# Performance work log

Hardware: AMD Instinct MI355X
Metric: run time of the kernel (lower is better)

The kernel has to match this reference:

```python
import jax, jax.numpy as jnp
import numpy as np

# fp4 e2m1 representable magnitudes and rounding midpoints
FP4_LEVELS = jnp.array([0.0, 0.5, 1.0, 1.5, 2.0, 3.0, 4.0, 6.0], dtype=jnp.float32)
FP4_BOUNDS = jnp.array([0.25, 0.75, 1.25, 1.75, 2.5, 3.5, 5.0], dtype=jnp.float32)
EPS = 1e-8
RANK = 64      # activation_lowrank_svd
NITER = 2      # activation_lowrank_niter


def fp4_get_scalar(x):
    # per-tensor scale: amax / max_fp4e2m1 (6.0)
    return jnp.maximum(jnp.max(jnp.abs(x)) / 6.0, EPS)


def fp4_qdq(x):
    # quant (round-to-nearest fp4e2m1 grid) followed by rquant (dequant)
    s = fp4_get_scalar(x)
    y = x / s
    a = jnp.clip(jnp.abs(y), 0.0, 6.0)
    idx = jnp.searchsorted(FP4_BOUNDS, a)  # nearest-level index
    return jnp.sign(y) * FP4_LEVELS[idx] * s


def power_iter_svd(G, V0, niter):
    # Dion-style power iteration: G ~ U diag(S) V^T, V0: [n,k]
    V = V0
    U = None
    W = None
    for it in range(niter):
        P = G @ V                                  # [m,k]
        U, _ = jnp.linalg.qr(P)                    # reduced QR, U: [m,k]
        W = G.T @ U                                # [n,k]
        if it < niter - 1:
            V = W / (jnp.linalg.norm(W, axis=0, keepdims=True) + EPS)
    S = jnp.linalg.norm(W, axis=0)                 # [k]
    Vn = W / (S[None, :] + EPS)                    # [n,k]
    return U, S, Vn


def svd_quant(x2d, V0):
    # low-rank kernel + fp4-quantized factors + fp4-quantized residual
    U, S, V = power_iter_svd(x2d, V0, NITER)
    ug = U.T                                       # [k,m]
    vg = V.T                                       # [k,n]
    ker = (U * S[None, :]) @ vg                    # [m,n] full-precision kernel
    ugq = fp4_qdq(ug)
    vgq = fp4_qdq(vg)
    res_q = fp4_qdq(x2d - ker)                     # quantized residual
    return (ugq.T * S[None, :]) @ vgq + res_q      # reconstructed input


def setup_inputs() -> dict:
    key = jax.random.key(0)
    k1, k2, k3, k4 = jax.random.split(key, 4)
    B, Sq, Din, Dout, R = 4, 2048, 4096, 4096, RANK
    x = jax.random.normal(k1, (B, Sq, Din), jnp.float32)
    weight = jax.random.normal(k2, (Dout, Din), jnp.float32) * (1.0 / np.sqrt(Din))
    bias = jax.random.normal(k3, (Dout,), jnp.float32) * 0.01
    V0 = jax.random.normal(k4, (Din, R), jnp.float32)  # cached subspace (state)
    return {"x": x, "weight": weight, "bias": bias, "V0": V0}


def reference(x, weight, bias, V0):
    B, Sq, Din = x.shape
    # activation SVD + fp4 quantization on flattened [B*S, Din]
    xq = svd_quant(x.reshape(-1, Din), V0).reshape(B, Sq, Din)
    # weight fp4 quant/dequant
    wq = fp4_qdq(weight)
    return xq @ wq.T + bias
```

## Files before the change

kernel.cpp:

```cpp
#include <hip/hip_runtime.h>
#include <stdint.h>

#define EPSF 1e-8f
#define KT 4160

typedef float  f32x4  __attribute__((ext_vector_type(4)));
typedef __bf16 bf16x8 __attribute__((ext_vector_type(8)));
typedef __bf16 bf16x4 __attribute__((ext_vector_type(4)));

constexpr size_t oP    = 0;
constexpr size_t oW    = oP  + 8192*64;
constexpr size_t oG    = oW  + 4096*64;
constexpr size_t oM1   = oG  + 64*64;
constexpr size_t oScal = oM1 + 64*4096;
constexpr size_t nZero1= oScal + 4;
constexpr size_t nZero2= oG + 64*64;
constexpr size_t oS    = nZero1;
constexpr size_t oLinv = oS + 64;
constexpr size_t oV    = oLinv + 64*64;
constexpr size_t oU    = oV + 4096*64;
constexpr size_t endF32= oU + 8192*64;
constexpr size_t bfByte= ((endF32*4 + 255)/256)*256;
constexpr size_t oVq   = 0;
constexpr size_t oA    = oVq + 64*4096;
constexpr size_t oB    = oA + (size_t)8192*4160;
constexpr size_t oVcT  = oB + (size_t)4096*4160;
constexpr size_t oUT   = oVcT + 3*(size_t)64*4096;
constexpr size_t oUhl  = oUT + 3*(size_t)64*8192;
constexpr size_t oKVT  = oUhl + 2*(size_t)8192*64;
constexpr size_t endBF = oKVT + 2*(size_t)4096*64;
constexpr size_t WS_NEED = bfByte + endBF*2;

__device__ __forceinline__ float qlevel(float a){
  if (a <= 0.25f) return 0.0f;
  if (a <= 0.75f) return 0.5f;
  if (a <= 1.25f) return 1.0f;
  if (a <= 1.75f) return 1.5f;
  if (a <= 2.5f)  return 2.0f;
  if (a <= 3.5f)  return 3.0f;
  if (a <= 5.0f)  return 4.0f;
  return 6.0f;
}
__device__ __forceinline__ float qgrid(float v, float s){
  float y = v / s;
  float l = qlevel(fabsf(y));
  return y < 0.0f ? -l : l;
}

__global__ void k_zero(float* p, int n){
  for (int i = blockIdx.x*blockDim.x + threadIdx.x; i < n; i += gridDim.x*blockDim.x)
    p[i] = 0.0f;
}

__global__ void k_amax4(const float4* __restrict__ x, int n4, unsigned* __restrict__ out){
  float m = 0.f;
  for (int i = blockIdx.x*blockDim.x + threadIdx.x; i < n4; i += gridDim.x*blockDim.x){
    float4 v = x[i];
    m = fmaxf(m, fmaxf(fmaxf(fabsf(v.x), fabsf(v.y)), fmaxf(fabsf(v.z), fabsf(v.w))));
  }
  for (int o = 32; o > 0; o >>= 1) m = fmaxf(m, __shfl_down(m, o, 64));
  __shared__ float sm[4];
  int lane = threadIdx.x & 63, w = threadIdx.x >> 6;
  if (lane == 0) sm[w] = m;
  __syncthreads();
  if (threadIdx.x == 0)
    atomicMax(out, __float_as_uint(fmaxf(fmaxf(sm[0],sm[1]), fmaxf(sm[2],sm[3]))));
}

__global__ __launch_bounds__(256) void k_gv(
    float* __restrict__ P, const float* __restrict__ x,
    const __bf16* __restrict__ Bh, const __bf16* __restrict__ Bm, const __bf16* __restrict__ Bl){
  int m0 = blockIdx.x * 128;
  int d0 = blockIdx.y * 512;
  int lane = threadIdx.x & 63, wave = threadIdx.x >> 6;
  int kgrp = lane >> 4, lrow = lane & 15;
  f32x4 acc[2][4] = {};
  for (int dc = d0; dc < d0 + 512; dc += 32){
    bf16x8 ah[2], am[2], al[2];
    #pragma unroll
    for (int f = 0; f < 2; f++){
      const float* g = x + (size_t)(m0 + wave*32 + f*16 + lrow)*4096 + dc + kgrp*8;
      float4 a = *(const float4*)g;
      float4 b = *(const float4*)(g + 4);
      float v[8] = {a.x,a.y,a.z,a.w,b.x,b.y,b.z,b.w};
      #pragma unroll
      for (int j = 0; j < 8; j++){
        __bf16 h = (__bf16)v[j];
        float r1 = v[j] - (float)h;
        __bf16 md = (__bf16)r1;
        float r2 = r1 - (float)md;
        ah[f][j] = h; am[f][j] = md; al[f][j] = (__bf16)r2;
      }
    }
    #pragma unroll
    for (int n = 0; n < 4; n++){
      size_t bo = (size_t)(n*16 + lrow)*4096 + dc + kgrp*8;
      bf16x8 bh = *(const bf16x8*)(Bh + bo);
      bf16x8 bm = *(const bf16x8*)(Bm + bo);
      bf16x8 bl = *(const bf16x8*)(Bl + bo);
      #pragma unroll
      for (int f = 0; f < 2; f++){
        acc[f][n] = __builtin_amdgcn_mfma_f32_16x16x32_bf16(ah[f], bh, acc[f][n],0,0,0);
        acc[f][n] = __builtin_amdgcn_mfma_f32_16x16x32_bf16(ah[f], bm, acc[f][n],0,0,0);
        acc[f][n] = __builtin_amdgcn_mfma_f32_16x16x32_bf16(am[f], bh, acc[f][n],0,0,0);
        acc[f][n] = __builtin_amdgcn_mfma_f32_16x16x32_bf16(ah[f], bl, acc[f][n],0,0,0);
        acc[f][n] = __builtin_amdgcn_mfma_f32_16x16x32_bf16(al[f], bh, acc[f][n],0,0,0);
        acc[f][n] = __builtin_amdgcn_mfma_f32_16x16x32_bf16(am[f], bm, acc[f][n],0,0,0);
      }
    }
  }
  #pragma unroll
  for (int f = 0; f < 2; f++)
    #pragma unroll
    for (int n = 0; n < 4; n++)
      #pragma unroll
      for (int r = 0; r < 4; r++)
        atomicAdd(&P[(size_t)(m0 + wave*32 + f*16 + kgrp*4 + r)*64 + n*16 + lrow], acc[f][n][r]);
}

__global__ __launch_bounds__(256) void k_gtu(
    float* __restrict__ W, const float* __restrict__ x,
    const __bf16* __restrict__ Bh, const __bf16* __restrict__ Bm, const __bf16* __restrict__ Bl){
  int d0 = blockIdx.x * 64;
  int m0 = blockIdx.y * 1024;
  int lane = threadIdx.x & 63, wave = threadIdx.x >> 6;
  int kgrp = lane >> 4, lrow = lane & 15;
  int dcol = d0 + wave*16 + lrow;
  f32x4 acc[4] = {};
  for (int mc = m0; mc < m0 + 1024; mc += 32){
    bf16x8 ah, am, al;
    int mb = mc + kgrp*8;
    #pragma unroll
    for (int j = 0; j < 8; j++){
      float v = x[(size_t)(mb + j)*4096 + dcol];
      __bf16 h = (__bf16)v;
      float r1 = v - (float)h;
      __bf16 md = (__bf16)r1;
      float r2 = r1 - (float)md;
      ah[j] = h; am[j] = md; al[j] = (__bf16)r2;
    }
    #pragma unroll
    for (int n = 0; n < 4; n++){
      size_t bo = (size_t)(n*16 + lrow)*8192 + mc + kgrp*8;
      bf16x8 bh = *(const bf16x8*)(Bh + bo);
      bf16x8 bm = *(const bf16x8*)(Bm + bo);
      bf16x8 bl = *(const bf16x8*)(Bl + bo);
      acc[n] = __builtin_amdgcn_mfma_f32_16x16x32_bf16(ah, bh, acc[n],0,0,0);
      acc[n] = __builtin_amdgcn_mfma_f32_16x16x32_bf16(ah, bm, acc[n],0,0,0);
      acc[n] = __builtin_amdgcn_mfma_f32_16x16x32_bf16(am, bh, acc[n],0,0,0);
      acc[n] = __builtin_amdgcn_mfma_f32_16x16x32_bf16(ah, bl, acc[n],0,0,0);
      acc[n] = __builtin_amdgcn_mfma_f32_16x16x32_bf16(al, bh, acc[n],0,0,0);
      acc[n] = __builtin_amdgcn_mfma_f32_16x16x32_bf16(am, bm, acc[n],0,0,0);
    }
  }
  #pragma unroll
  for (int n = 0; n < 4; n++)
    #pragma unroll
    for (int r = 0; r < 4; r++)
      atomicAdd(&W[(size_t)(d0 + wave*16 + kgrp*4 + r)*64 + n*16 + lrow], acc[n][r]);
}

__global__ void k_gram(const float* __restrict__ P, float* __restrict__ Gram){
  __shared__ float Pt[128][65];
  int m0 = blockIdx.x * 128;
  int t = threadIdx.x;
  for (int i = 0; i < 32; i++){
    int idx = i*256 + t; int r = idx >> 6, c = idx & 63;
    Pt[r][c] = P[(size_t)(m0+r)*64 + c];
  }
  __syncthreads();
  int ti = t >> 4, tj = t & 15;
  float acc[4][4] = {};
  for (int r = 0; r < 128; r++){
    float a[4], b[4];
    #pragma unroll
    for (int q = 0; q < 4; q++) a[q] = Pt[r][ti*4+q];
    #pragma unroll
    for (int q = 0; q < 4; q++) b[q] = Pt[r][tj*4+q];
    #pragma unroll
    for (int xx = 0; xx < 4; xx++)
      #pragma unroll
      for (int y = 0; y < 4; y++) acc[xx][y] += a[xx]*b[y];
  }
  for (int xx = 0; xx < 4; xx++)
    for (int y = 0; y < 4; y++)
      atomicAdd(&Gram[(ti*4+xx)*64 + tj*4+y], acc[xx][y]);
}

__global__ void k_cholinv(const float* __restrict__ Gram, float* __restrict__ Linv){
  __shared__ double A[64][64];
  __shared__ double Li[64][64];
  int t = threadIdx.x;
  for (int j = 0; j < 64; j++){ A[t][j] = (double)Gram[t*64+j]; Li[t][j] = 0.0; }
  __syncthreads();
  for (int k = 0; k < 64; k++){
    if (t == k) A[k][k] = sqrt(A[k][k]);
    __syncthreads();
    if (t > k) A[t][k] /= A[k][k];
    __syncthreads();
    if (t > k){
      double aik = A[t][k];
      for (int j = k+1; j <= t; j++) A[t][j] -= aik * A[j][k];
    }
    __syncthreads();
  }
  for (int i = t; i < 64; i++){
    double s = (i == t) ? 1.0 : 0.0;
    for (int p = t; p < i; p++) s -= A[i][p] * Li[p][t];
    Li[i][t] = s / A[i][i];
  }
  __syncthreads();
  for (int j = 0; j < 64; j++) Linv[t*64+j] = (float)Li[t][j];
}

__global__ void k_applyq(float* __restrict__ U, const float* __restrict__ P,
                         const float* __restrict__ Linv){
  __shared__ float Pt[64][65];
  __shared__ float Lt[64][65];
  int m0 = blockIdx.x * 64;
  int t = threadIdx.x;
  for (int i = 0; i < 16; i++){
    int idx = i*256 + t; int r = idx >> 6, c = idx & 63;
    Pt[r][c] = P[(size_t)(m0+r)*64 + c];
    Lt[r][c] = Linv[r*64 + c];
  }
  __syncthreads();
  int tm = t >> 4, tj = t & 15;
  float acc[4][4] = {};
  for (int i = 0; i < 64; i++){
    float p[4], lv[4];
    #pragma unroll
    for (int a = 0; a < 4; a++) p[a]  = Pt[tm*4+a][i];
    #pragma unroll
    for (int b = 0; b < 4; b++) lv[b] = Lt[tj*4+b][i];
    #pragma unroll
    for (int a = 0; a < 4; a++)
      #pragma unroll
      for (int b = 0; b < 4; b++) acc[a][b] += p[a]*lv[b];
  }
  for (int a = 0; a < 4; a++)
    for (int b = 0; b < 4; b++)
      U[(size_t)(m0+tm*4+a)*64 + tj*4+b] = acc[a][b];
}

__global__ void k_colnorm(const float* __restrict__ W, float* __restrict__ cn){
  int k = blockIdx.x;
  float s = 0.f;
  for (int d = threadIdx.x; d < 4096; d += 256){
    float v = W[(size_t)d*64 + k];
    s += v*v;
  }
  for (int o = 32; o > 0; o >>= 1) s += __shfl_down(s, o, 64);
  __shared__ float sm[4];
  int lane = threadIdx.x & 63, w = threadIdx.x >> 6;
  if (lane == 0) sm[w] = s;
  __syncthreads();
  if (threadIdx.x == 0) cn[k] = sqrtf(sm[0]+sm[1]+sm[2]+sm[3]);
}

__global__ void k_vnorm(float* __restrict__ V, const float* __restrict__ W,
                        const float* __restrict__ cn){
  int i = blockIdx.x*256 + threadIdx.x;
  int k = i & 63;
  V[i] = W[i] / (cn[k] + EPSF);
}

__global__ void k_vnkv(float* __restrict__ V, __bf16* __restrict__ Kh, __bf16* __restrict__ Kl,
                       const float* __restrict__ W, const float* __restrict__ S,
                       unsigned* __restrict__ amaxv){
  int i = blockIdx.x*256 + threadIdx.x;
  int k = i & 63, d = i >> 6;
  float s = S[k];
  float vn = W[i] / (s + EPSF);
  V[i] = vn;
  float kv = s * vn;
  __bf16 h = (__bf16)kv;
  Kh[(size_t)d*64 + k] = h;
  Kl[(size_t)d*64 + k] = (__bf16)(kv - (float)h);
  float m = fabsf(vn);
  for (int o = 32; o > 0; o >>= 1) m = fmaxf(m, __shfl_down(m, o, 64));
  __shared__ float sm[4];
  int lane = threadIdx.x & 63, w = threadIdx.x >> 6;
  if (lane == 0) sm[w] = m;
  __syncthreads();
  if (threadIdx.x == 0)
    atomicMax(amaxv, __float_as_uint(fmaxf(fmaxf(sm[0],sm[1]), fmaxf(sm[2],sm[3]))));
}

__global__ void k_prep_vct(const float* __restrict__ Vc, __bf16* __restrict__ Th,
                           __bf16* __restrict__ Tm, __bf16* __restrict__ Tl){
  __shared__ float Vt[64][65];
  int d0 = blockIdx.x * 64;
  int t = threadIdx.x;
  for (int i = 0; i < 16; i++){
    int idx = i*256 + t; int r = idx >> 6, c = idx & 63;
    Vt[r][c] = Vc[(size_t)(d0 + r)*64 + c];
  }
  __syncthreads();
  for (int i = 0; i < 16; i++){
    int idx = i*256 + t; int k = idx >> 6, dd = idx & 63;
    float v = Vt[dd][k];
    __bf16 h = (__bf16)v;
    float r1 = v - (float)h;
    __bf16 md = (__bf16)r1;
    float r2 = r1 - (float)md;
    size_t o = (size_t)k*4096 + d0 + dd;
    Th[o] = h; Tm[o] = md; Tl[o] = (__bf16)r2;
  }
}

__global__ void k_prep_u(const float* __restrict__ Ub, __bf16* __restrict__ Uh, __bf16* __restrict__ Ul,
                         __bf16* __restrict__ Th, __bf16* __restrict__ Tm, __bf16* __restrict__ Tl){
  __shared__ float Ut[64][65];
  int m0 = blockIdx.x * 64;
  int t = threadIdx.x;
  for (int i = 0; i < 16; i++){
    int idx = i*256 + t; int r = idx >> 6, c = idx & 63;
    float v = Ub[(size_t)(m0 + r)*64 + c];
    Ut[r][c] = v;
    __bf16 h = (__bf16)v;
    Uh[(size_t)(m0+r)*64 + c] = h;
    Ul[(size_t)(m0+r)*64 + c] = (__bf16)(v - (float)h);
  }
  __syncthreads();
  for (int i = 0; i < 16; i++){
    int idx = i*256 + t; int k = idx >> 6, mm = idx & 63;
    float v = Ut[mm][k];
    __bf16 h = (__bf16)v;
    float r1 = v - (float)h;
    __bf16 md = (__bf16)r1;
    float r2 = r1 - (float)md;
    size_t o = (size_t)k*8192 + m0 + mm;
    Th[o] = h; Tm[o] = md; Tl[o] = (__bf16)r2;
  }
}

__global__ void k_qw(__bf16* __restrict__ Bq, const float* __restrict__ w,
                     const unsigned* __restrict__ amaxw){
  float s = fmaxf(__uint_as_float(*amaxw) / 6.0f, EPSF);
  int i = blockIdx.x*256 + threadIdx.x;
  int n = i >> 10, d = (i & 1023)*4;
  float4 v = *(const float4*)(w + (size_t)n*4096 + d);
  bf16x4 o;
  o[0] = (__bf16)qgrid(v.x, s); o[1] = (__bf16)qgrid(v.y, s);
  o[2] = (__bf16)qgrid(v.z, s); o[3] = (__bf16)qgrid(v.w, s);
  *(bf16x4*)(Bq + (size_t)n*4160 + d) = o;
}

__global__ void k_qu(__bf16* __restrict__ Aq, const float* __restrict__ U,
                     const unsigned* __restrict__ amaxu){
  float s = fmaxf(__uint_as_float(*amaxu) / 6.0f, EPSF);
  int i = blockIdx.x*256 + threadIdx.x;
  int m = i >> 6, k = i & 63;
  Aq[(size_t)m*4160 + 4096 + k] = (__bf16)qgrid(U[i], s);
}

__global__ void k_qv(__bf16* __restrict__ Vq, const float* __restrict__ V,
                     const unsigned* __restrict__ amaxv){
  __shared__ float Vt[64][65];
  float s = fmaxf(__uint_as_float(*amaxv)/6.0f, EPSF);
  int d0 = blockIdx.x * 64;
  int t = threadIdx.x;
  for (int i = 0; i < 16; i++){
    int idx = i*256 + t; int r = idx >> 6, c = idx & 63;
    Vt[r][c] = V[(size_t)(d0 + r)*64 + c];
  }
  __syncthreads();
  for (int i = 0; i < 16; i++){
    int idx = i*256 + t; int k = idx >> 6, dd = idx & 63;
    Vq[(size_t)k*4096 + d0 + dd] = (__bf16)qgrid(Vt[dd][k], s);
  }
}

__global__ __launch_bounds__(256) void k_res(
    const float* __restrict__ x, const __bf16* __restrict__ Uh, const __bf16* __restrict__ Ul,
    const __bf16* __restrict__ Kh, const __bf16* __restrict__ Kl,
    unsigned* __restrict__ amaxr, __bf16* __restrict__ Aq, int mode){
  int m0 = blockIdx.x * 64, n0 = blockIdx.y * 128;
  int lane = threadIdx.x & 63, wave = threadIdx.x >> 6;
  int kgrp = lane >> 4, lrow = lane & 15;
  int mrow = m0 + wave*16 + lrow;
  f32x4 acc[8] = {};
  #pragma unroll
  for (int ks = 0; ks < 2; ks++){
    size_t ao = (size_t)mrow*64 + ks*32 + kgrp*8;
    bf16x8 uh = *(const bf16x8*)(Uh + ao);
    bf16x8 ul = *(const bf16x8*)(Ul + ao);
    #pragma unroll
    for (int n = 0; n < 8; n++){
      size_t bo = (size_t)(n0 + n*16 + lrow)*64 + ks*32 + kgrp*8;
      bf16x8 kh = *(const bf16x8*)(Kh + bo);
      bf16x8 kl = *(const bf16x8*)(Kl + bo);
      acc[n] = __builtin_amdgcn_mfma_f32_16x16x32_bf16(uh, kh, acc[n],0,0,0);
      acc[n] = __builtin_amdgcn_mfma_f32_16x16x32_bf16(uh, kl, acc[n],0,0,0);
      acc[n] = __builtin_amdgcn_mfma_f32_16x16x32_bf16(ul, kh, acc[n],0,0,0);
    }
  }
  int mb = m0 + wave*16 + kgrp*4;
  if (mode == 0){
    float mx = 0.f;
    #pragma unroll
    for (int n = 0; n < 8; n++){
      int c = n0 + n*16 + lrow;
      #pragma unroll
      for (int r = 0; r < 4; r++)
        mx = fmaxf(mx, fabsf(x[(size_t)(mb + r)*4096 + c] - acc[n][r]));
    }
    for (int o = 32; o > 0; o >>= 1) mx = fmaxf(mx, __shfl_down(mx, o, 64));
    __shared__ float sm[4];
    if (lane == 0) sm[wave] = mx;
    __syncthreads();
    if (threadIdx.x == 0)
      atomicMax(amaxr, __float_as_uint(fmaxf(fmaxf(sm[0],sm[1]), fmaxf(sm[2],sm[3]))));
  } else {
    float s = fmaxf(__uint_as_float(*amaxr)/6.0f, EPSF);
    #pragma unroll
    for (int n = 0; n < 8; n++){
      int c = n0 + n*16 + lrow;
      #pragma unroll
      for (int r = 0; r < 4; r++)
        Aq[(size_t)(mb + r)*4160 + c] =
          (__bf16)qgrid(x[(size_t)(mb + r)*4096 + c] - acc[n][r], s);
    }
  }
}

__global__ __launch_bounds__(256) void k_m1(
    float* __restrict__ M1g, const __bf16* __restrict__ Vq, const __bf16* __restrict__ Bq){
  int n0 = blockIdx.x * 64;
  int k0 = blockIdx.y * 512;
  int lane = threadIdx.x & 63, wave = threadIdx.x >> 6;
  int kgrp = lane >> 4, lrow = lane & 15;
  int nrow = n0 + wave*16 + lrow;
  f32x4 acc[4] = {};
  for (int kc = k0; kc < k0 + 512; kc += 32){
    bf16x8 fb = *(const bf16x8*)(Bq + (size_t)nrow*4160 + kc + kgrp*8);
    #pragma unroll
    for (int mt = 0; mt < 4; mt++){
      bf16x8 fa = *(const bf16x8*)(Vq + (size_t)(mt*16 + lrow)*4096 + kc + kgrp*8);
      acc[mt] = __builtin_amdgcn_mfma_f32_16x16x32_bf16(fa, fb, acc[mt],0,0,0);
    }
  }
  #pragma unroll
  for (int mt = 0; mt < 4; mt++)
    #pragma unroll
    for (int r = 0; r < 4; r++)
      atomicAdd(&M1g[(size_t)(mt*16 + kgrp*4 + r)*4096 + nrow], acc[mt][r]);
}

__global__ void k_m2t(__bf16* __restrict__ Bq, const float* __restrict__ M1g,
                      const float* __restrict__ S, const unsigned* __restrict__ scal){
  float su = fmaxf(__uint_as_float(scal[1])/6.0f, EPSF);
  float sv = fmaxf(__uint_as_float(scal[2])/6.0f, EPSF);
  float sr = fmaxf(__uint_as_float(scal[3])/6.0f, EPSF);
  int i = blockIdx.x*256 + threadIdx.x;
  int n = i >> 6, k = i & 63;
  float v = M1g[(size_t)k*4096 + n] * (su * sv * S[k] / sr);
  Bq[(size_t)n*4160 + 4096 + k] = (__bf16)v;
}

__global__ __launch_bounds__(512, 2)
void k_gemm(float* __restrict__ out, const __bf16* __restrict__ A,
            const __bf16* __restrict__ B, const float* __restrict__ bias,
            const unsigned* __restrict__ scal){
  __shared__ __align__(16) __bf16 As[4*8192];
  __shared__ __align__(16) __bf16 Bs[4*8192];
  const int m0 = blockIdx.y * 256, n0 = blockIdx.x * 256;
  const int tid = threadIdx.x;
  const int lane = tid & 63, wave = tid >> 6;
  const int wrow = wave >> 2, wcol = wave & 3;
  const int kg = lane >> 4, lr = lane & 15;
  f32x4 acc[8][4] = {};

  auto STAGE = [&](int tt){
    __bf16* as = &As[(tt & 3) * 8192];
    __bf16* bs = &Bs[(tt & 3) * 8192];
    const int kt = tt * 32;
    #pragma unroll
    for (int q = 0; q < 2; q++){
      int idx = q * 512 + tid;
      int rp  = idx >> 3;
      int sp  = (idx & 7) ^ (rp & 7);
      int grow = rp * 2 + (sp >> 2);
      int gcol = (sp & 3) * 8;
      const __bf16* ga = A + (size_t)(m0 + grow) * KT + kt + gcol;
      const __bf16* gb = B + (size_t)(n0 + grow) * KT + kt + gcol;
      __bf16* la = as + (size_t)(idx & ~63) * 8;
      __bf16* lb = bs + (size_t)(idx & ~63) * 8;
      __builtin_amdgcn_global_load_lds((const __attribute__((address_space(1))) uint32_t*)ga,
                                       (__attribute__((address_space(3))) uint32_t*)la, 16, 0, 0);
      __builtin_amdgcn_global_load_lds((const __attribute__((address_space(1))) uint32_t*)gb,
                                       (__attribute__((address_space(3))) uint32_t*)lb, 16, 0, 0);
    }
  };

  auto BODY = [&](int t, bool stage){
    const __bf16* as = &As[(t & 3) * 8192];
    const __bf16* bs = &Bs[(t & 3) * 8192];
    bf16x8 fa[8], fb[4];
    #pragma unroll
    for (int mf = 0; mf < 8; mf++){
      int row = wrow*128 + mf*16 + lr;
      int rp  = row >> 1;
      int sl  = (((row & 1) << 2) | kg) ^ (rp & 7);
      fa[mf] = *(const bf16x8*)(as + (size_t)rp*64 + sl*8);
    }
    #pragma unroll
    for (int nf = 0; nf < 4; nf++){
      int row = wcol*64 + nf*16 + lr;
      int rp  = row >> 1;
      int sl  = (((row & 1) << 2) | kg) ^ (rp & 7);
      fb[nf] = *(const bf16x8*)(bs + (size_t)rp*64 + sl*8);
    }
    if (stage) STAGE(t + 3);
    __builtin_amdgcn_s_setprio(1);
    #pragma unroll
    for (int mf = 0; mf < 8; mf++)
      #pragma unroll
      for (int nf = 0; nf < 4; nf++)
        acc[mf][nf] = __builtin_amdgcn_mfma_f32_16x16x32_bf16(fa[mf], fb[nf], acc[mf][nf], 0, 0, 0);
    __builtin_amdgcn_s_setprio(0);
  };

  STAGE(0); STAGE(1); STAGE(2);

  const int NT = KT / 32;
  for (int t = 0; t < NT - 2; t++){
    asm volatile("s_waitcnt vmcnt(8)" ::: "memory");
    __builtin_amdgcn_s_barrier();
    BODY(t, t < NT - 3);
  }
  asm volatile("s_waitcnt vmcnt(4)" ::: "memory");
  __builtin_amdgcn_s_barrier();
  BODY(NT - 2, false);
  asm volatile("s_waitcnt vmcnt(0)" ::: "memory");
  __builtin_amdgcn_s_barrier();
  BODY(NT - 1, false);

  float sr = fmaxf(__uint_as_float(scal[3])/6.0f, EPSF);
  float sw = fmaxf(__uint_as_float(scal[0])/6.0f, EPSF);
  float srw = sr * sw;
  #pragma unroll
  for (int nf = 0; nf < 4; nf++){
    int n = n0 + wcol*64 + nf*16 + lr;
    float bv = bias[n];
    #pragma unroll
    for (int mf = 0; mf < 8; mf++){
      int mb = m0 + wrow*128 + mf*16 + 4*kg;
      #pragma unroll
      for (int r = 0; r < 4; r++)
        out[(size_t)(mb + r)*4096 + n] = acc[mf][nf][r]*srw + bv;
    }
  }
}

extern "C" void kernel_launch(void* const* d_in, const int* in_sizes, int n_in,
                              void* d_out, int out_size, void* d_ws, size_t ws_size,
                              hipStream_t stream){
  const float* x    = (const float*)d_in[0];
  const float* wt   = (const float*)d_in[1];
  const float* bias = (const float*)d_in[2];
  const float* V0   = (const float*)d_in[3];
  float* out = (float*)d_out;
  if (ws_size < WS_NEED) return;

  float* F = (float*)d_ws;
  unsigned* scal = (unsigned*)(F + oScal);
  __bf16* BFp = (__bf16*)((char*)d_ws + bfByte);
  __bf16* Vq  = BFp + oVq;
  __bf16* Aq  = BFp + oA;
  __bf16* Bq  = BFp + oB;
  __bf16* VcTh = BFp + oVcT,              *VcTm = VcTh + (size_t)64*4096, *VcTl = VcTm + (size_t)64*4096;
  __bf16* UTh  = BFp + oUT,               *UTm  = UTh + (size_t)64*8192,  *UTl  = UTm + (size_t)64*8192;
  __bf16* Uh   = BFp + oUhl,              *Ul   = Uh + (size_t)8192*64;
  __bf16* KVTh = BFp + oKVT,              *KVTl = KVTh + (size_t)4096*64;
  float *P = F+oP, *W = F+oW, *Gm = F+oG, *M1 = F+oM1, *Sv = F+oS,
        *Li = F+oLinv, *V = F+oV, *Ub = F+oU;

  dim3 b256(256);
  k_zero <<<dim3(2048), b256, 0, stream>>>(F, (int)nZero1);
  k_amax4<<<dim3(1024), b256, 0, stream>>>((const float4*)wt, 4194304, scal+0);
  k_qw   <<<dim3(16384), b256, 0, stream>>>(Bq, wt, scal+0);

  k_prep_vct<<<dim3(64),  b256, 0, stream>>>(V0, VcTh, VcTm, VcTl);
  k_gv     <<<dim3(64,8), b256, 0, stream>>>(P, x, VcTh, VcTm, VcTl);
  k_gram   <<<dim3(64),   b256, 0, stream>>>(P, Gm);
  k_cholinv<<<dim3(1), dim3(64), 0, stream>>>(Gm, Li);
  k_applyq <<<dim3(128),  b256, 0, stream>>>(Ub, P, Li);
  k_prep_u <<<dim3(128),  b256, 0, stream>>>(Ub, Uh, Ul, UTh, UTm, UTl);
  k_gtu    <<<dim3(64,8), b256, 0, stream>>>(W, x, UTh, UTm, UTl);
  k_colnorm<<<dim3(64),   b256, 0, stream>>>(W, Sv);
  k_vnorm  <<<dim3(1024), b256, 0, stream>>>(V, W, Sv);

  k_prep_vct<<<dim3(64),  b256, 0, stream>>>(V, VcTh, VcTm, VcTl);
  k_zero   <<<dim3(2048), b256, 0, stream>>>(F, (int)nZero2);
  k_gv     <<<dim3(64,8), b256, 0, stream>>>(P, x, VcTh, VcTm, VcTl);
  k_gram   <<<dim3(64),   b256, 0, stream>>>(P, Gm);
  k_cholinv<<<dim3(1), dim3(64), 0, stream>>>(Gm, Li);
  k_applyq <<<dim3(128),  b256, 0, stream>>>(Ub, P, Li);
  k_prep_u <<<dim3(128),  b256, 0, stream>>>(Ub, Uh, Ul, UTh, UTm, UTl);
  k_gtu    <<<dim3(64,8), b256, 0, stream>>>(W, x, UTh, UTm, UTl);
  k_colnorm<<<dim3(64),   b256, 0, stream>>>(W, Sv);
  k_vnkv   <<<dim3(1024), b256, 0, stream>>>(V, KVTh, KVTl, W, Sv, scal+2);

  k_amax4<<<dim3(1024), b256, 0, stream>>>((const float4*)Ub, 131072, scal+1);
  k_qu   <<<dim3(2048), b256, 0, stream>>>(Aq, Ub, scal+1);
  k_qv   <<<dim3(64),   b256, 0, stream>>>(Vq, V, scal+2);
  k_res  <<<dim3(128,32), b256, 0, stream>>>(x, Uh, Ul, KVTh, KVTl, scal+3, Aq, 0);
  k_res  <<<dim3(128,32), b256, 0, stream>>>(x, Uh, Ul, KVTh, KVTl, scal+3, Aq, 1);

  k_m1  <<<dim3(64,8), b256, 0, stream>>>(M1, Vq, Bq);
  k_m2t <<<dim3(1024), b256, 0, stream>>>(Bq, M1, Sv, scal);
  k_gemm<<<dim3(16,32), dim3(512), 0, stream>>>(out, Aq, Bq, bias, scal);
}
```

Before: 1.515 ms.

## Replace atomic split-K reductions with partial buffers, fuse normalization, swizzle GEMM tiles

```diff
diff --git a/kernel.cpp b/kernel.cpp
--- a/kernel.cpp
+++ b/kernel.cpp
@@ -13,9 +13,8 @@
 constexpr size_t oG    = oW  + 4096*64;
 constexpr size_t oM1   = oG  + 64*64;
 constexpr size_t oScal = oM1 + 64*4096;
-constexpr size_t nZero1= oScal + 4;
-constexpr size_t nZero2= oG + 64*64;
-constexpr size_t oS    = nZero1;
+constexpr size_t nZeroA= 64*64 + 64*4096 + 4;
+constexpr size_t oS    = oScal + 4;
 constexpr size_t oLinv = oS + 64;
 constexpr size_t oV    = oLinv + 64*64;
 constexpr size_t oU    = oV + 4096*64;
@@ -68,10 +67,11 @@
 }
 
 __global__ __launch_bounds__(256) void k_gv(
-    float* __restrict__ P, const float* __restrict__ x,
+    float* __restrict__ P8, const float* __restrict__ x,
     const __bf16* __restrict__ Bh, const __bf16* __restrict__ Bm, const __bf16* __restrict__ Bl){
   int m0 = blockIdx.x * 128;
   int d0 = blockIdx.y * 512;
+  size_t pb = (size_t)blockIdx.y * 8192 * 64;
   int lane = threadIdx.x & 63, wave = threadIdx.x >> 6;
   int kgrp = lane >> 4, lrow = lane & 15;
   f32x4 acc[2][4] = {};
@@ -115,14 +115,15 @@
     for (int n = 0; n < 4; n++)
       #pragma unroll
       for (int r = 0; r < 4; r++)
-        atomicAdd(&P[(size_t)(m0 + wave*32 + f*16 + kgrp*4 + r)*64 + n*16 + lrow], acc[f][n][r]);
+        P8[pb + (size_t)(m0 + wave*32 + f*16 + kgrp*4 + r)*64 + n*16 + lrow] = acc[f][n][r];
 }
 
 __global__ __launch_bounds__(256) void k_gtu(
-    float* __restrict__ W, const float* __restrict__ x,
+    float* __restrict__ W8, const float* __restrict__ x,
     const __bf16* __restrict__ Bh, const __bf16* __restrict__ Bm, const __bf16* __restrict__ Bl){
   int d0 = blockIdx.x * 64;
   int m0 = blockIdx.y * 1024;
+  size_t wb = (size_t)blockIdx.y * 4096 * 64;
   int lane = threadIdx.x & 63, wave = threadIdx.x >> 6;
   int kgrp = lane >> 4, lrow = lane & 15;
   int dcol = d0 + wave*16 + lrow;
@@ -157,16 +158,22 @@
   for (int n = 0; n < 4; n++)
     #pragma unroll
     for (int r = 0; r < 4; r++)
-      atomicAdd(&W[(size_t)(d0 + wave*16 + kgrp*4 + r)*64 + n*16 + lrow], acc[n][r]);
-}
-
-__global__ void k_gram(const float* __restrict__ P, float* __restrict__ Gram){
+      W8[wb + (size_t)(d0 + wave*16 + kgrp*4 + r)*64 + n*16 + lrow] = acc[n][r];
+}
+
+__global__ void k_gram(const float* __restrict__ P8, float* __restrict__ Psum,
+                       float* __restrict__ Gram){
   __shared__ float Pt[128][65];
   int m0 = blockIdx.x * 128;
   int t = threadIdx.x;
   for (int i = 0; i < 32; i++){
     int idx = i*256 + t; int r = idx >> 6, c = idx & 63;
-    Pt[r][c] = P[(size_t)(m0+r)*64 + c];
+    float s = 0.f;
+    #pragma unroll
+    for (int b = 0; b < 8; b++)
+      s += P8[((size_t)b*8192 + m0 + r)*64 + c];
+    Pt[r][c] = s;
+    Psum[(size_t)(m0+r)*64 + c] = s;
   }
   __syncthreads();
   int ti = t >> 4, tj = t & 15;
@@ -243,11 +250,16 @@
       U[(size_t)(m0+tm*4+a)*64 + tj*4+b] = acc[a][b];
 }
 
-__global__ void k_colnorm(const float* __restrict__ W, float* __restrict__ cn){
+__global__ void k_colnorm(const float* __restrict__ W8, float* __restrict__ Wsum,
+                          float* __restrict__ cn){
   int k = blockIdx.x;
   float s = 0.f;
   for (int d = threadIdx.x; d < 4096; d += 256){
-    float v = W[(size_t)d*64 + k];
+    float v = 0.f;
+    #pragma unroll
+    for (int b = 0; b < 8; b++)
+      v += W8[((size_t)b*4096 + d)*64 + k];
+    Wsum[(size_t)d*64 + k] = v;
     s += v*v;
   }
   for (int o = 32; o > 0; o >>= 1) s += __shfl_down(s, o, 64);
@@ -258,21 +270,13 @@
   if (threadIdx.x == 0) cn[k] = sqrtf(sm[0]+sm[1]+sm[2]+sm[3]);
 }
 
-__global__ void k_vnorm(float* __restrict__ V, const float* __restrict__ W,
-                        const float* __restrict__ cn){
-  int i = blockIdx.x*256 + threadIdx.x;
-  int k = i & 63;
-  V[i] = W[i] / (cn[k] + EPSF);
-}
-
-__global__ void k_vnkv(float* __restrict__ V, __bf16* __restrict__ Kh, __bf16* __restrict__ Kl,
-                       const float* __restrict__ W, const float* __restrict__ S,
-                       unsigned* __restrict__ amaxv){
+__global__ void k_kv(__bf16* __restrict__ Kh, __bf16* __restrict__ Kl,
+                     const float* __restrict__ W, const float* __restrict__ S,
+                     unsigned* __restrict__ amaxv){
   int i = blockIdx.x*256 + threadIdx.x;
   int k = i & 63, d = i >> 6;
   float s = S[k];
   float vn = W[i] / (s + EPSF);
-  V[i] = vn;
   float kv = s * vn;
   __bf16 h = (__bf16)kv;
   Kh[(size_t)d*64 + k] = h;
@@ -295,6 +299,32 @@
   for (int i = 0; i < 16; i++){
     int idx = i*256 + t; int r = idx >> 6, c = idx & 63;
     Vt[r][c] = Vc[(size_t)(d0 + r)*64 + c];
+  }
+  __syncthreads();
+  for (int i = 0; i < 16; i++){
+    int idx = i*256 + t; int k = idx >> 6, dd = idx & 63;
+    float v = Vt[dd][k];
+    __bf16 h = (__bf16)v;
+    float r1 = v - (float)h;
+    __bf16 md = (__bf16)r1;
+    float r2 = r1 - (float)md;
+    size_t o = (size_t)k*4096 + d0 + dd;
+    Th[o] = h; Tm[o] = md; Tl[o] = (__bf16)r2;
+  }
+}
+
+__global__ void k_prep_vctn(const float* __restrict__ W, const float* __restrict__ cn,
+                            __bf16* __restrict__ Th, __bf16* __restrict__ Tm,
+                            __bf16* __restrict__ Tl){
+  __shared__ float Vt[64][65];
+  __shared__ float cs[64];
+  int d0 = blockIdx.x * 64;
+  int t = threadIdx.x;
+  if (t < 64) cs[t] = cn[t];
+  __syncthreads();
+  for (int i = 0; i < 16; i++){
+    int idx = i*256 + t; int r = idx >> 6, c = idx & 63;
+    Vt[r][c] = W[(size_t)(d0 + r)*64 + c] / (cs[c] + EPSF);
   }
   __syncthreads();
   for (int i = 0; i < 16; i++){
@@ -355,15 +385,18 @@
   Aq[(size_t)m*4160 + 4096 + k] = (__bf16)qgrid(U[i], s);
 }
 
-__global__ void k_qv(__bf16* __restrict__ Vq, const float* __restrict__ V,
-                     const unsigned* __restrict__ amaxv){
+__global__ void k_qv(__bf16* __restrict__ Vq, const float* __restrict__ W,
+                     const float* __restrict__ S, const unsigned* __restrict__ amaxv){
   __shared__ float Vt[64][65];
+  __shared__ float cs[64];
   float s = fmaxf(__uint_as_float(*amaxv)/6.0f, EPSF);
   int d0 = blockIdx.x * 64;
   int t = threadIdx.x;
+  if (t < 64) cs[t] = S[t];
+  __syncthreads();
   for (int i = 0; i < 16; i++){
     int idx = i*256 + t; int r = idx >> 6, c = idx & 63;
-    Vt[r][c] = V[(size_t)(d0 + r)*64 + c];
+    Vt[r][c] = W[(size_t)(d0 + r)*64 + c] / (cs[c] + EPSF);
   }
   __syncthreads();
   for (int i = 0; i < 16; i++){
@@ -465,7 +498,9 @@
             const unsigned* __restrict__ scal){
   __shared__ __align__(16) __bf16 As[4*8192];
   __shared__ __align__(16) __bf16 Bs[4*8192];
-  const int m0 = blockIdx.y * 256, n0 = blockIdx.x * 256;
+  const int bid = blockIdx.y * gridDim.x + blockIdx.x;
+  const int wg  = (bid & 7) * 64 + (bid >> 3);
+  const int m0 = (wg & 31) * 256, n0 = (wg >> 5) * 256;
   const int tid = threadIdx.x;
   const int lane = tid & 63, wave = tid >> 6;
   const int wrow = wave >> 2, wcol = wave & 3;
@@ -495,9 +530,17 @@
   };
 
   auto BODY = [&](int t, bool stage){
+    if (stage) STAGE(t + 3);
     const __bf16* as = &As[(t & 3) * 8192];
     const __bf16* bs = &Bs[(t & 3) * 8192];
     bf16x8 fa[8], fb[4];
+    #pragma unroll
+    for (int nf = 0; nf < 4; nf++){
+      int row = wcol*64 + nf*16 + lr;
+      int rp  = row >> 1;
+      int sl  = (((row & 1) << 2) | kg) ^ (rp & 7);
+      fb[nf] = *(const bf16x8*)(bs + (size_t)rp*64 + sl*8);
+    }
     #pragma unroll
     for (int mf = 0; mf < 8; mf++){
       int row = wrow*128 + mf*16 + lr;
@@ -505,14 +548,6 @@
       int sl  = (((row & 1) << 2) | kg) ^ (rp & 7);
       fa[mf] = *(const bf16x8*)(as + (size_t)rp*64 + sl*8);
     }
-    #pragma unroll
-    for (int nf = 0; nf < 4; nf++){
-      int row = wcol*64 + nf*16 + lr;
-      int rp  = row >> 1;
-      int sl  = (((row & 1) << 2) | kg) ^ (rp & 7);
-      fb[nf] = *(const bf16x8*)(bs + (size_t)rp*64 + sl*8);
-    }
-    if (stage) STAGE(t + 3);
     __builtin_amdgcn_s_setprio(1);
     #pragma unroll
     for (int mf = 0; mf < 8; mf++)
@@ -575,37 +610,38 @@
   __bf16* Uh   = BFp + oUhl,              *Ul   = Uh + (size_t)8192*64;
   __bf16* KVTh = BFp + oKVT,              *KVTl = KVTh + (size_t)4096*64;
   float *P = F+oP, *W = F+oW, *Gm = F+oG, *M1 = F+oM1, *Sv = F+oS,
-        *Li = F+oLinv, *V = F+oV, *Ub = F+oU;
+        *Li = F+oLinv, *Ub = F+oU;
+  float* P8 = (float*)Aq;
+  float* W8 = P8 + (size_t)8*8192*64;
 
   dim3 b256(256);
-  k_zero <<<dim3(2048), b256, 0, stream>>>(F, (int)nZero1);
+  k_zero <<<dim3(512),  b256, 0, stream>>>(F + oG, (int)nZeroA);
   k_amax4<<<dim3(1024), b256, 0, stream>>>((const float4*)wt, 4194304, scal+0);
   k_qw   <<<dim3(16384), b256, 0, stream>>>(Bq, wt, scal+0);
 
   k_prep_vct<<<dim3(64),  b256, 0, stream>>>(V0, VcTh, VcTm, VcTl);
-  k_gv     <<<dim3(64,8), b256, 0, stream>>>(P, x, VcTh, VcTm, VcTl);
-  k_gram   <<<dim3(64),   b256, 0, stream>>>(P, Gm);
+  k_gv     <<<dim3(64,8), b256, 0, stream>>>(P8, x, VcTh, VcTm, VcTl);
+  k_gram   <<<dim3(64),   b256, 0, stream>>>(P8, P, Gm);
   k_cholinv<<<dim3(1), dim3(64), 0, stream>>>(Gm, Li);
   k_applyq <<<dim3(128),  b256, 0, stream>>>(Ub, P, Li);
   k_prep_u <<<dim3(128),  b256, 0, stream>>>(Ub, Uh, Ul, UTh, UTm, UTl);
-  k_gtu    <<<dim3(64,8), b256, 0, stream>>>(W, x, UTh, UTm, UTl);
-  k_colnorm<<<dim3(64),   b256, 0, stream>>>(W, Sv);
-  k_vnorm  <<<dim3(1024), b256, 0, stream>>>(V, W, Sv);
-
-  k_prep_vct<<<dim3(64),  b256, 0, stream>>>(V, VcTh, VcTm, VcTl);
-  k_zero   <<<dim3(2048), b256, 0, stream>>>(F, (int)nZero2);
-  k_gv     <<<dim3(64,8), b256, 0, stream>>>(P, x, VcTh, VcTm, VcTl);
-  k_gram   <<<dim3(64),   b256, 0, stream>>>(P, Gm);
+  k_gtu    <<<dim3(64,8), b256, 0, stream>>>(W8, x, UTh, UTm, UTl);
+  k_colnorm<<<dim3(64),   b256, 0, stream>>>(W8, W, Sv);
+  k_prep_vctn<<<dim3(64), b256, 0, stream>>>(W, Sv, VcTh, VcTm, VcTl);
+
+  k_zero   <<<dim3(64),   b256, 0, stream>>>(Gm, 4096);
+  k_gv     <<<dim3(64,8), b256, 0, stream>>>(P8, x, VcTh, VcTm, VcTl);
+  k_gram   <<<dim3(64),   b256, 0, stream>>>(P8, P, Gm);
   k_cholinv<<<dim3(1), dim3(64), 0, stream>>>(Gm, Li);
   k_applyq <<<dim3(128),  b256, 0, stream>>>(Ub, P, Li);
   k_prep_u <<<dim3(128),  b256, 0, stream>>>(Ub, Uh, Ul, UTh, UTm, UTl);
-  k_gtu    <<<dim3(64,8), b256, 0, stream>>>(W, x, UTh, UTm, UTl);
-  k_colnorm<<<dim3(64),   b256, 0, stream>>>(W, Sv);
-  k_vnkv   <<<dim3(1024), b256, 0, stream>>>(V, KVTh, KVTl, W, Sv, scal+2);
+  k_gtu    <<<dim3(64,8), b256, 0, stream>>>(W8, x, UTh, UTm, UTl);
+  k_colnorm<<<dim3(64),   b256, 0, stream>>>(W8, W, Sv);
+  k_kv     <<<dim3(1024), b256, 0, stream>>>(KVTh, KVTl, W, Sv, scal+2);
 
   k_amax4<<<dim3(1024), b256, 0, stream>>>((const float4*)Ub, 131072, scal+1);
   k_qu   <<<dim3(2048), b256, 0, stream>>>(Aq, Ub, scal+1);
-  k_qv   <<<dim3(64),   b256, 0, stream>>>(Vq, V, scal+2);
+  k_qv   <<<dim3(64),   b256, 0, stream>>>(Vq, W, Sv, scal+2);
   k_res  <<<dim3(128,32), b256, 0, stream>>>(x, Uh, Ul, KVTh, KVTl, scal+3, Aq, 0);
   k_res  <<<dim3(128,32), b256, 0, stream>>>(x, Uh, Ul, KVTh, KVTl, scal+3, Aq, 1);
 
```

New measurement: 1.695 ms. 1.12x slower.
